# Optimization experiments

Hardware: AMD Instinct MI355X
Metric: run time of the kernel (lower is better)

Reference implementation:

```python
import jax, jax.numpy as jnp
import numpy as np

IN, OUT, HID = 64, 32, 256
B, T = 64, 256
NOISE_STD, TAU = 0.05, 0.2


def setup_inputs() -> dict:
    key = jax.random.key(0)
    ks = jax.random.split(key, 8)
    u = jax.random.normal(ks[0], (B, T, IN), dtype=jnp.float32)
    x0 = jax.random.normal(ks[1], (B, HID), dtype=jnp.float32)
    noise = jax.random.normal(ks[2], (T, B, HID), dtype=jnp.float32)
    w_hh_rnn = jax.random.normal(ks[3], (HID, HID), dtype=jnp.float32) * (0.1 / HID ** 0.5)
    w_hh_tbrnn = jax.random.normal(ks[4], (HID, HID, HID), dtype=jnp.float32) * (0.1 / HID)
    w_in_w = jax.random.normal(ks[5], (HID, IN), dtype=jnp.float32)
    w_in_b = jnp.zeros((HID,), dtype=jnp.float32)
    w_out_w = jax.random.normal(ks[6], (OUT, HID), dtype=jnp.float32) * 4.0
    w_out_b = jax.random.normal(ks[7], (OUT,), dtype=jnp.float32) * 0.0
    return {"u": u, "x0": x0, "noise": noise, "w_hh_rnn": w_hh_rnn,
            "w_hh_tbrnn": w_hh_tbrnn, "w_in_w": w_in_w, "w_in_b": w_in_b,
            "w_out_w": w_out_w, "w_out_b": w_out_b}


def reference(u, x0, noise, w_hh_rnn, w_hh_tbrnn, w_in_w, w_in_b, w_out_w, w_out_b):
    # mode='cont', form='rate', adv=False, nonlinearity=tanh, output_nonlinearity=tanh
    u_t_first = jnp.transpose(u, (1, 0, 2))  # [T, B, IN]

    def step(x, inp):
        u_t, n_t = inp
        r = jnp.tanh(x)                                   # rate form
        input_I = u_t @ w_in_w.T + w_in_b                 # [B, HID]
        hidden_W1 = r @ w_hh_rnn.T                        # [B, HID]
        # out[b,j] = sum_{i,k} r[b,i] * W[j,i,k] * r[b,k]
        hidden_W2 = jnp.einsum('bi,jik,bk->bj', r, w_hh_tbrnn, r)
        rec_x = hidden_W1 + hidden_W2 + input_I
        x_new = x + NOISE_STD * n_t + TAU * (-x + rec_x)  # cont mode
        return x_new, x_new

    x_final, traj = jax.lax.scan(step, x0, (u_t_first, noise))
    trajectories = jnp.transpose(traj, (1, 0, 2))         # [B, T, HID]
    output = jnp.tanh(trajectories) @ w_out_w.T + w_out_b  # [B, T, OUT]
    return output, x_final, trajectories
```

## Files before the change

### kernel.cpp

```cpp
#include <hip/hip_runtime.h>
#include <hip/hip_bf16.h>
#include <math.h>

#define HID 256
#define BSZ 64
#define TLEN 256
#define INW 64
#define OUTW 32
#define NOISE_STD 0.05f
#define TAU 0.2f

typedef __attribute__((ext_vector_type(8))) short short8;
typedef __attribute__((ext_vector_type(4))) float floatx4;
typedef unsigned long long u64;

__device__ __forceinline__ int ridx(int b, int k) {
    int P = ((b >> 2) & 7) ^ ((b & 3) << 1);
    return b * 256 + ((((k >> 3) ^ P) & 31) << 3) + (k & 7);
}

__global__ __launch_bounds__(256) void swizzle_kernel(const float* __restrict__ W,
                                                      __hip_bfloat16* __restrict__ Wsw) {
    int g = blockIdx.x * 256 + threadIdx.x;
    int l  = g & 63;
    int ni = (g >> 6) & 15;
    int kk = (g >> 10) & 7;
    int j  = g >> 13;
    int i  = ni * 16 + (l & 15);
    int k0 = kk * 32 + (l >> 4) * 8;
    const float* __restrict__ src = W + ((size_t)j * HID + i) * HID + k0;
    __hip_bfloat16* __restrict__ dst = Wsw + (size_t)g * 8;
#pragma unroll
    for (int e = 0; e < 8; ++e) dst[e] = __float2bfloat16(src[e]);
}

__global__ __launch_bounds__(256) void init_kernel(const float* __restrict__ x0,
                                                   u64* __restrict__ buf0) {
    int g = blockIdx.x;
    int k = threadIdx.x;
    u64 v = 0;
#pragma unroll
    for (int e = 0; e < 4; ++e) {
        __hip_bfloat16 h = __float2bfloat16(tanhf(x0[(4 * g + e) * HID + k]));
        v |= (u64)(*(unsigned short*)&h) << (16 * e);
    }
    buf0[g * 256 + k] = v;
}

__global__ __launch_bounds__(256) void pre_kernel(const float* __restrict__ u,
                                                  const float* __restrict__ w_in_w,
                                                  const float* __restrict__ w_in_b,
                                                  const float* __restrict__ noise,
                                                  float* __restrict__ pre) {
    __shared__ float ulds[BSZ][INW + 4];
    const int t = blockIdx.x;
    const int j = threadIdx.x;
    {
        int b = threadIdx.x >> 2, q = threadIdx.x & 3;
#pragma unroll
        for (int e = 0; e < 4; ++e) {
            float4 v = *(const float4*)(u + ((size_t)b * TLEN + t) * INW + q * 16 + e * 4);
            *(float4*)&ulds[b][q * 16 + e * 4] = v;
        }
    }
    float wreg[INW];
#pragma unroll
    for (int q = 0; q < INW / 4; ++q) {
        float4 v = *(const float4*)(w_in_w + (size_t)j * INW + q * 4);
        wreg[q * 4 + 0] = v.x; wreg[q * 4 + 1] = v.y;
        wreg[q * 4 + 2] = v.z; wreg[q * 4 + 3] = v.w;
    }
    float bias = w_in_b[j];
    __syncthreads();
    for (int b = 0; b < BSZ; ++b) {
        float s = bias;
#pragma unroll
        for (int in_ = 0; in_ < INW; ++in_) s = fmaf(ulds[b][in_], wreg[in_], s);
        float nz = noise[((size_t)t * BSZ + b) * HID + j];
        pre[((size_t)t * HID + j) * BSZ + b] = NOISE_STD * nz + TAU * s;
    }
}

__global__ __launch_bounds__(256, 1) void persist_kernel(
    const __hip_bfloat16* __restrict__ Wsw,
    const float* __restrict__ w_hh,
    const float* __restrict__ u,
    const float* __restrict__ w_in_w,
    const float* __restrict__ w_in_b,
    const float* __restrict__ noise,
    const float* __restrict__ x0,
    u64* __restrict__ buf0,
    u64* __restrict__ buf1,
    float* __restrict__ traj,
    float* __restrict__ trajWS,
    float* __restrict__ xfinal,
    int* __restrict__ ready,
    const float* __restrict__ pre,
    int use_pre, int use_tws) {
    __shared__ short rlds[16384];
    __shared__ float redw[256];
    __shared__ char lds_pad[57344];

    const int tid  = threadIdx.x;
    const int j    = blockIdx.x;
    const int w    = tid >> 6;
    const int lane = tid & 63;
    const int quad = lane >> 4;
    const int col  = lane & 15;

    if (j == 0x7fffffff) lds_pad[tid] = 0;

    short8 wreg[32];
    {
        const short* __restrict__ wsh = (const short*)Wsw;
#pragma unroll
        for (int kk = 0; kk < 8; ++kk)
#pragma unroll
            for (int nj = 0; nj < 4; ++nj)
                wreg[kk * 4 + nj] = *(const short8*)(wsh +
                    ((((size_t)j * 8 + kk) * 16 + (w * 4 + nj)) * 64 + lane) * 8);
    }
    float whh_reg[4];
#pragma unroll
    for (int nj = 0; nj < 4; ++nj)
        whh_reg[nj] = w_hh[j * HID + (w * 4 + nj) * 16 + col];

    float xb = 0.f;
    if (tid < BSZ) xb = x0[tid * HID + j];

#pragma unroll 1
    for (int t = 0; t < TLEN; ++t) {
        const u64* __restrict__ rcur = (t & 1) ? buf1 : buf0;
        u64* __restrict__ rnxt = (t & 1) ? buf0 : buf1;

        float extra = 0.f;
        if (tid < BSZ) {
            if (use_pre) {
                extra = pre[((size_t)t * HID + j) * BSZ + tid];
            } else {
                float isum = w_in_b[j];
                const float4* __restrict__ urow =
                    (const float4*)(u + ((size_t)tid * TLEN + t) * INW);
                const float4* __restrict__ wrow = (const float4*)(w_in_w + (size_t)j * INW);
#pragma unroll
                for (int q = 0; q < INW / 4; ++q) {
                    float4 uu = urow[q], ww = wrow[q];
                    isum = fmaf(uu.x, ww.x, isum);
                    isum = fmaf(uu.y, ww.y, isum);
                    isum = fmaf(uu.z, ww.z, isum);
                    isum = fmaf(uu.w, ww.w, isum);
                }
                float nz = noise[((size_t)t * BSZ + tid) * HID + j];
                extra = NOISE_STD * nz + TAU * isum;
            }
        }

        if (t > 0) {
            while (__hip_atomic_load(ready + tid * 16, __ATOMIC_RELAXED,
                                     __HIP_MEMORY_SCOPE_AGENT) < t)
                __builtin_amdgcn_s_sleep(1);
            asm volatile("" ::: "memory");
        }

        {
            u64 v[16];
#pragma unroll
            for (int g = 0; g < 16; ++g)
                v[g] = __hip_atomic_load(rcur + g * 256 + tid, __ATOMIC_RELAXED,
                                         __HIP_MEMORY_SCOPE_AGENT);
#pragma unroll
            for (int g = 0; g < 16; ++g)
#pragma unroll
                for (int e = 0; e < 4; ++e)
                    rlds[ridx(4 * g + e, tid)] = (short)(v[g] >> (16 * e));
        }
        __syncthreads();

        floatx4 acc[4][4];
#pragma unroll
        for (int mb = 0; mb < 4; ++mb)
#pragma unroll
            for (int nj = 0; nj < 4; ++nj) acc[mb][nj] = (floatx4){0.f, 0.f, 0.f, 0.f};

#pragma unroll
        for (int kk = 0; kk < 8; ++kk) {
            short8 afrag[4];
#pragma unroll
            for (int mb = 0; mb < 4; ++mb)
                afrag[mb] = *(const short8*)&rlds[ridx(mb * 16 + col, kk * 32 + quad * 8)];
#pragma unroll
            for (int nj = 0; nj < 4; ++nj)
#pragma unroll
                for (int mb = 0; mb < 4; ++mb)
                    acc[mb][nj] = __builtin_amdgcn_mfma_f32_16x16x32_bf16(
                        afrag[mb], wreg[kk * 4 + nj], acc[mb][nj], 0, 0, 0);
        }

        float part[16];
#pragma unroll
        for (int p = 0; p < 16; ++p) part[p] = 0.f;
#pragma unroll
        for (int nj = 0; nj < 4; ++nj) {
            int i = (w * 4 + nj) * 16 + col;
            float whh = whh_reg[nj];
#pragma unroll
            for (int mb = 0; mb < 4; ++mb)
#pragma unroll
                for (int reg = 0; reg < 4; ++reg) {
                    int b = mb * 16 + quad * 4 + reg;
                    short rs = rlds[ridx(b, i)];
                    float rv = __bfloat162float(*(__hip_bfloat16*)&rs);
                    part[mb * 4 + reg] = fmaf(rv, acc[mb][nj][reg] + whh, part[mb * 4 + reg]);
                }
        }
#pragma unroll
        for (int s = 1; s < 16; s <<= 1) {
#pragma unroll
            for (int p = 0; p < 16; ++p) part[p] += __shfl_xor(part[p], s, 64);
        }
        if (col == 0) {
#pragma unroll
            for (int mb = 0; mb < 4; ++mb)
#pragma unroll
                for (int reg = 0; reg < 4; ++reg)
                    redw[w * 64 + mb * 16 + quad * 4 + reg] = part[mb * 4 + reg];
        }
        __syncthreads();

        if (w == 0) {
            const int b = lane;
            float rec = redw[b] + redw[64 + b] + redw[128 + b] + redw[192 + b];
            float xn = xb + extra + TAU * (rec - xb);
            xb = xn;

            if (t < TLEN - 1) {
                __hip_bfloat16 h = __float2bfloat16(tanhf(xn));
                int hs = (int)(*(unsigned short*)&h);
                int src = 4 * (lane & 15);
                u64 pv = (u64)(unsigned)__shfl(hs, src + 0, 64)
                       | ((u64)(unsigned)__shfl(hs, src + 1, 64) << 16)
                       | ((u64)(unsigned)__shfl(hs, src + 2, 64) << 32)
                       | ((u64)(unsigned)__shfl(hs, src + 3, 64) << 48);
                if (lane < 16)
                    __hip_atomic_store(rnxt + (size_t)lane * 256 + j, pv,
                                       __ATOMIC_RELAXED, __HIP_MEMORY_SCOPE_AGENT);
                asm volatile("s_waitcnt vmcnt(0)" ::: "memory");
                if (lane == 0)
                    __hip_atomic_store(ready + j * 16, t + 1, __ATOMIC_RELAXED,
                                       __HIP_MEMORY_SCOPE_AGENT);
            }

            if (use_tws) {
                trajWS[((size_t)t * HID + j) * BSZ + b] = xn;
            } else {
                traj[((size_t)b * TLEN + t) * HID + j] = xn;
                if (t == TLEN - 1) xfinal[b * HID + j] = xn;
            }
        }
    }
}

__global__ __launch_bounds__(256) void fixup_kernel(
    const float* __restrict__ trajWS,
    const float* __restrict__ w_out_w,
    const float* __restrict__ w_out_b,
    float* __restrict__ traj,
    float* __restrict__ xfinal,
    float* __restrict__ out) {
    __shared__ float xv[BSZ * 257];
    __shared__ float wol[OUTW * 257];
    const int t = blockIdx.x, tid = threadIdx.x;

#pragma unroll
    for (int it = 0; it < 16; ++it) {
        int flat = it * 1024 + tid * 4;
        float4 v = *(const float4*)(trajWS + (size_t)t * 16384 + flat);
        int jj = flat >> 6, b = flat & 63;
        xv[(b + 0) * 257 + jj] = v.x;
        xv[(b + 1) * 257 + jj] = v.y;
        xv[(b + 2) * 257 + jj] = v.z;
        xv[(b + 3) * 257 + jj] = v.w;
    }
#pragma unroll
    for (int it = 0; it < 8; ++it) {
        int flat = it * 1024 + tid * 4;
        float4 v = *(const float4*)(w_out_w + flat);
        int o = flat >> 8, h = flat & 255;
        *(float4*)&wol[o * 257 + h] = v;
    }
    __syncthreads();

    for (int b = 0; b < BSZ; ++b)
        traj[((size_t)b * TLEN + t) * HID + tid] = xv[b * 257 + tid];
    if (t == TLEN - 1)
        for (int b = 0; b < BSZ; ++b)
            xfinal[b * HID + tid] = xv[b * 257 + tid];

    __syncthreads();
#pragma unroll
    for (int it = 0; it < 64; ++it)
        xv[it * 257 + tid] = tanhf(xv[it * 257 + tid]);
    __syncthreads();

    const int o = tid & 31;
    const float bias = w_out_b[o];
#pragma unroll 1
    for (int rep = 0; rep < 8; ++rep) {
        int b = rep * 8 + (tid >> 5);
        float s = bias;
#pragma unroll 8
        for (int h = 0; h < HID; ++h)
            s = fmaf(xv[b * 257 + h], wol[o * 257 + h], s);
        out[((size_t)b * TLEN + t) * OUTW + o] = s;
    }
}

__global__ __launch_bounds__(256) void output_kernel(
    const float* __restrict__ traj, const float* __restrict__ w_out_w,
    const float* __restrict__ w_out_b, float* __restrict__ out) {
    __shared__ float th[8][HID + 1];
    const int bt0 = blockIdx.x * 8;
    const int tid = threadIdx.x;
#pragma unroll
    for (int m = 0; m < 8; ++m) {
        int idx = m * 256 + tid;
        th[idx >> 8][idx & 255] = tanhf(traj[(size_t)bt0 * HID + idx]);
    }
    __syncthreads();
    const int row = tid >> 5, o = tid & 31;
    const float* __restrict__ wrow = w_out_w + (size_t)o * HID;
    float s = w_out_b[o];
#pragma unroll 8
    for (int h = 0; h < HID; ++h) s = fmaf(th[row][h], wrow[h], s);
    out[(size_t)(bt0 + row) * OUTW + o] = s;
}

extern "C" void kernel_launch(void* const* d_in, const int* in_sizes, int n_in,
                              void* d_out, int out_size, void* d_ws, size_t ws_size,
                              hipStream_t stream) {
    const float* u       = (const float*)d_in[0];
    const float* x0      = (const float*)d_in[1];
    const float* noise   = (const float*)d_in[2];
    const float* w_hh    = (const float*)d_in[3];
    const float* W       = (const float*)d_in[4];
    const float* w_in_w  = (const float*)d_in[5];
    const float* w_in_b  = (const float*)d_in[6];
    const float* w_out_w = (const float*)d_in[7];
    const float* w_out_b = (const float*)d_in[8];

    float* out    = (float*)d_out;
    float* xfinal = out + (size_t)BSZ * TLEN * OUTW;
    float* traj   = xfinal + (size_t)BSZ * HID;

    char* ws = (char*)d_ws;
    __hip_bfloat16* Wsw = (__hip_bfloat16*)ws;
    u64*   buf0 = (u64*)(ws + 33554432);
    u64*   buf1 = (u64*)(ws + 33587200);
    int*   rdy  = (int*)(ws + 33619968);
    float* tws  = (float*)(ws + 33636352);
    float* pre  = (float*)(ws + 50413568);
    const size_t NEED_TWS = 50413568ull;
    const size_t NEED_PRE = 67190784ull;
    const int use_tws = (ws_size >= NEED_TWS) ? 1 : 0;
    const int use_pre = (ws_size >= NEED_PRE) ? 1 : 0;

    hipMemsetAsync(rdy, 0, 16384, stream);
    swizzle_kernel<<<8192, 256, 0, stream>>>(W, Wsw);
    init_kernel<<<16, 256, 0, stream>>>(x0, buf0);
    if (use_pre)
        pre_kernel<<<TLEN, 256, 0, stream>>>(u, w_in_w, w_in_b, noise, pre);

    persist_kernel<<<256, 256, 0, stream>>>(
        Wsw, w_hh, u, w_in_w, w_in_b, noise, x0,
        buf0, buf1, traj, tws, xfinal, rdy, pre, use_pre, use_tws);

    if (use_tws)
        fixup_kernel<<<TLEN, 256, 0, stream>>>(tws, w_out_w, w_out_b, traj, xfinal, out);
    else
        output_kernel<<<(BSZ * TLEN) / 8, 256, 0, stream>>>(traj, w_out_w, w_out_b, out);
}
```

Before: 1.611 ms.

## Tag recurrent-state packets with step number and drop producer store fence

The per-step exchange of bf16 tanh(x) values now packs three batch values plus a 16-bit step tag into each 64-bit packet. Consumers spin on each packet's tag until it matches the current step. This lets the producer drop the s_waitcnt vmcnt(0) fence between writing packets and raising the ready flag, removing a store-drain stall from the critical recurrence path. The cost is 22 packets instead of 16, so more global loads and stores per step. The LDS padding that forced one block per CU is also removed, which could change how blocks are placed on CUs.

```diff
diff --git a/kernel.cpp b/kernel.cpp
--- a/kernel.cpp
+++ b/kernel.cpp
@@ -9,6 +9,7 @@
 #define OUTW 32
 #define NOISE_STD 0.05f
 #define TAU 0.2f
+#define NPKT 22
 
 typedef __attribute__((ext_vector_type(8))) short short8;
 typedef __attribute__((ext_vector_type(4))) float floatx4;
@@ -36,15 +37,18 @@
 
 __global__ __launch_bounds__(256) void init_kernel(const float* __restrict__ x0,
                                                    u64* __restrict__ buf0) {
-    int g = blockIdx.x;
+    int c = blockIdx.x;
     int k = threadIdx.x;
     u64 v = 0;
 #pragma unroll
-    for (int e = 0; e < 4; ++e) {
-        __hip_bfloat16 h = __float2bfloat16(tanhf(x0[(4 * g + e) * HID + k]));
-        v |= (u64)(*(unsigned short*)&h) << (16 * e);
-    }
-    buf0[g * 256 + k] = v;
+    for (int e = 0; e < 3; ++e) {
+        int b = 3 * c + e;
+        if (b < BSZ) {
+            __hip_bfloat16 h = __float2bfloat16(tanhf(x0[b * HID + k]));
+            v |= (u64)(*(unsigned short*)&h) << (16 * e);
+        }
+    }
+    buf0[c * 256 + k] = v;
 }
 
 __global__ __launch_bounds__(256) void pre_kernel(const float* __restrict__ u,
@@ -99,7 +103,6 @@
     int use_pre, int use_tws) {
     __shared__ short rlds[16384];
     __shared__ float redw[256];
-    __shared__ char lds_pad[57344];
 
     const int tid  = threadIdx.x;
     const int j    = blockIdx.x;
@@ -107,8 +110,6 @@
     const int lane = tid & 63;
     const int quad = lane >> 4;
     const int col  = lane & 15;
-
-    if (j == 0x7fffffff) lds_pad[tid] = 0;
 
     short8 wreg[32];
     {
@@ -162,18 +163,26 @@
             asm volatile("" ::: "memory");
         }
 
-        {
-            u64 v[16];
-#pragma unroll
-            for (int g = 0; g < 16; ++g)
-                v[g] = __hip_atomic_load(rcur + g * 256 + tid, __ATOMIC_RELAXED,
+        u64 v[NPKT];
+#pragma unroll
+        for (int c = 0; c < NPKT; ++c)
+            v[c] = __hip_atomic_load(rcur + c * 256 + tid, __ATOMIC_RELAXED,
+                                     __HIP_MEMORY_SCOPE_AGENT);
+#pragma unroll
+        for (int c = 0; c < NPKT; ++c) {
+            while ((unsigned)(v[c] >> 48) != (unsigned)(t & 0xFFFF)) {
+                __builtin_amdgcn_s_sleep(1);
+                v[c] = __hip_atomic_load(rcur + c * 256 + tid, __ATOMIC_RELAXED,
                                          __HIP_MEMORY_SCOPE_AGENT);
-#pragma unroll
-            for (int g = 0; g < 16; ++g)
-#pragma unroll
-                for (int e = 0; e < 4; ++e)
-                    rlds[ridx(4 * g + e, tid)] = (short)(v[g] >> (16 * e));
-        }
+            }
+        }
+
+#pragma unroll
+        for (int c = 0; c < NPKT - 1; ++c)
+#pragma unroll
+            for (int e = 0; e < 3; ++e)
+                rlds[ridx(3 * c + e, tid)] = (short)(v[c] >> (16 * e));
+        rlds[ridx(63, tid)] = (short)v[NPKT - 1];
         __syncthreads();
 
         floatx4 acc[4][4];
@@ -236,15 +245,14 @@
             if (t < TLEN - 1) {
                 __hip_bfloat16 h = __float2bfloat16(tanhf(xn));
                 int hs = (int)(*(unsigned short*)&h);
-                int src = 4 * (lane & 15);
-                u64 pv = (u64)(unsigned)__shfl(hs, src + 0, 64)
-                       | ((u64)(unsigned)__shfl(hs, src + 1, 64) << 16)
-                       | ((u64)(unsigned)__shfl(hs, src + 2, 64) << 32)
-                       | ((u64)(unsigned)__shfl(hs, src + 3, 64) << 48);
-                if (lane < 16)
+                int src = 3 * lane;
+                u64 pv = (u64)(unsigned)(unsigned short)__shfl(hs, src + 0, 64)
+                       | ((u64)(unsigned)(unsigned short)__shfl(hs, src + 1, 64) << 16)
+                       | ((u64)(unsigned)(unsigned short)__shfl(hs, src + 2, 64) << 32)
+                       | ((u64)(unsigned)((t + 1) & 0xFFFF) << 48);
+                if (lane < NPKT)
                     __hip_atomic_store(rnxt + (size_t)lane * 256 + j, pv,
                                        __ATOMIC_RELAXED, __HIP_MEMORY_SCOPE_AGENT);
-                asm volatile("s_waitcnt vmcnt(0)" ::: "memory");
                 if (lane == 0)
                     __hip_atomic_store(ready + j * 16, t + 1, __ATOMIC_RELAXED,
                                        __HIP_MEMORY_SCOPE_AGENT);
@@ -355,18 +363,18 @@
     char* ws = (char*)d_ws;
     __hip_bfloat16* Wsw = (__hip_bfloat16*)ws;
     u64*   buf0 = (u64*)(ws + 33554432);
-    u64*   buf1 = (u64*)(ws + 33587200);
-    int*   rdy  = (int*)(ws + 33619968);
-    float* tws  = (float*)(ws + 33636352);
-    float* pre  = (float*)(ws + 50413568);
-    const size_t NEED_TWS = 50413568ull;
-    const size_t NEED_PRE = 67190784ull;
+    u64*   buf1 = (u64*)(ws + 33599488);
+    int*   rdy  = (int*)(ws + 33644544);
+    float* tws  = (float*)(ws + 33660928);
+    float* pre  = (float*)(ws + 50438144);
+    const size_t NEED_TWS = 50438144ull;
+    const size_t NEED_PRE = 67215360ull;
     const int use_tws = (ws_size >= NEED_TWS) ? 1 : 0;
     const int use_pre = (ws_size >= NEED_PRE) ? 1 : 0;
 
     hipMemsetAsync(rdy, 0, 16384, stream);
     swizzle_kernel<<<8192, 256, 0, stream>>>(W, Wsw);
-    init_kernel<<<16, 256, 0, stream>>>(x0, buf0);
+    init_kernel<<<NPKT, 256, 0, stream>>>(x0, buf0);
     if (use_pre)
         pre_kernel<<<TLEN, 256, 0, stream>>>(u, w_in_w, w_in_b, noise, pre);
 
```

Measured after the change: 2.114 ms. 31.2% more time.
